# Kernel tuning notes

Measured on AMD Instinct MI355X. Metric: run time of the kernel, lower is better.

Reference implementation:

```python
import jax, jax.numpy as jnp
import numpy as np

HIDDEN = 1024
EMBED = HIDDEN // 4
SEQ = 512
BATCH = 256
NUM_CLASSES = 10


def setup_inputs() -> dict:
    key = jax.random.key(0)
    ks = jax.random.split(key, 16)

    def w(k, d1, d2):
        # kaiming_normal_ with nonlinearity='linear': std = 1/sqrt(fan_in=d2)
        return jax.random.normal(k, (d1, d2), dtype=jnp.float32) / jnp.sqrt(d2)

    inp = {
        "x": jax.random.randint(ks[0], (BATCH, SEQ), 0, 3),
        "emb": jax.random.normal(ks[1], (3, EMBED), dtype=jnp.float32),
        "w_gx": w(ks[2], EMBED, HIDDEN), "w_gh": w(ks[3], HIDDEN, HIDDEN), "b_g": jnp.zeros((HIDDEN,), jnp.float32),
        "w_ix": w(ks[4], EMBED, HIDDEN), "w_ih": w(ks[5], HIDDEN, HIDDEN), "b_i": jnp.zeros((HIDDEN,), jnp.float32),
        "w_fx": w(ks[6], EMBED, HIDDEN), "w_fh": w(ks[7], HIDDEN, HIDDEN), "b_f": jnp.zeros((HIDDEN,), jnp.float32),
        "w_ox": w(ks[8], EMBED, HIDDEN), "w_oh": w(ks[9], HIDDEN, HIDDEN), "b_o": jnp.zeros((HIDDEN,), jnp.float32),
        "w_ph": w(ks[10], HIDDEN, NUM_CLASSES), "b_p": jnp.zeros((NUM_CLASSES,), jnp.float32),
    }
    return inp


def reference(x, emb, w_gx, w_gh, b_g, w_ix, w_ih, b_i, w_fx, w_fh, b_f,
              w_ox, w_oh, b_o, w_ph, b_p):
    B, T = x.shape
    embedded = emb[x]                         # [B, T, E]
    pad = ((x + 1) // 2).astype(emb.dtype)    # [B, T]

    xs = (jnp.swapaxes(embedded, 0, 1),       # [T, B, E]
          jnp.swapaxes(pad, 0, 1))            # [T, B]

    h0 = jnp.zeros((B, w_gh.shape[0]), emb.dtype)
    c0 = jnp.zeros_like(h0)

    def step(carry, inputs):
        h, c = carry
        xt, pt = inputs
        g = jnp.tanh(xt @ w_gx + h @ w_gh + b_g)
        i = jax.nn.sigmoid(xt @ w_ix + h @ w_ih + b_i)
        f = jax.nn.sigmoid(xt @ w_fx + h @ w_fh + b_f)
        o = jax.nn.sigmoid(xt @ w_ox + h @ w_oh + b_o)
        c = g * i + c * f
        h = jnp.tanh(c) * o
        c = c * pt[:, None]
        return (h, c), None

    (h, _), _ = jax.lax.scan(step, (h0, c0), xs)
    p = h @ w_ph + b_p                        # [B, num_classes]
    # Faithful to original: log_softmax over dim=0 (batch dim)
    return jax.nn.log_softmax(p, axis=0)
```

## Files before the change

kernel.cpp:

```cpp
#include <hip/hip_runtime.h>
#include <hip/hip_bf16.h>

#define T_SEQ 512
#define BATCH 256
#define HID   1024
#define EMBD  256
#define NCLS  10

typedef __bf16 bf16x8 __attribute__((ext_vector_type(8)));
typedef float  floatx16 __attribute__((ext_vector_type(16)));
typedef float  floatx2 __attribute__((ext_vector_type(2)));
typedef unsigned short ushortx8 __attribute__((ext_vector_type(8)));

__device__ __forceinline__ unsigned int f2bf(float f) {
    unsigned int u = __builtin_bit_cast(unsigned int, f);
    u += 0x7fffu + ((u >> 16) & 1u);
    return u >> 16;
}
__device__ __forceinline__ float sig_fast(float x) {
    return __builtin_amdgcn_rcpf(1.0f + __expf(-x));
}
__device__ __forceinline__ float tanh_fast(float x) {
    return 1.0f - 2.0f * __builtin_amdgcn_rcpf(1.0f + __expf(2.0f * x));
}

__global__ void prep_xw_kernel(const float* __restrict__ emb,
                               const float* __restrict__ wgx, const float* __restrict__ wix,
                               const float* __restrict__ wfx, const float* __restrict__ wox,
                               const float* __restrict__ bg,  const float* __restrict__ bi,
                               const float* __restrict__ bf,  const float* __restrict__ bo,
                               float* __restrict__ XW) {
    int gid = blockIdx.x * blockDim.x + threadIdx.x;
    if (gid >= 3 * 4 * HID) return;
    int tok  = gid >> 12;
    int gate = (gid >> 10) & 3;
    int n    = gid & 1023;
    const float* W = gate == 0 ? wgx : gate == 1 ? wix : gate == 2 ? wfx : wox;
    const float* B = gate == 0 ? bg  : gate == 1 ? bi  : gate == 2 ? bf  : bo;
    float acc = B[n];
    const float* e = emb + tok * EMBD;
    for (int k = 0; k < EMBD; ++k) acc += e[k] * W[k * HID + n];
    XW[gid] = acc;
}

__global__ void prep_w_kernel(const float* __restrict__ wgh, const float* __restrict__ wih,
                              const float* __restrict__ wfh, const float* __restrict__ woh,
                              unsigned short* __restrict__ Wt) {
    int bid = blockIdx.x;
    int w   = bid & 31;
    int i   = (bid >> 5) & 15;
    int q   = (bid >> 9) & 3;
    int g   = bid >> 11;
    const float* W = g == 0 ? wgh : g == 1 ? wih : g == 2 ? wfh : woh;
    int lane = threadIdx.x;
    int j    = w * 32 + (lane & 31);
    int k0   = q * 256 + i * 16 + (lane >> 5) * 8;
    ushortx8 o8;
    #pragma unroll
    for (int e = 0; e < 8; ++e) o8[e] = (unsigned short)f2bf(W[(k0 + e) * HID + j]);
    int frag = ((w * 4 + g) * 4 + q) * 16 + i;
    *(ushortx8*)&Wt[frag * 512 + lane * 8] = o8;
}

__global__ __launch_bounds__(512, 2)
void lstm_kernel(const int* __restrict__ x, const float* __restrict__ XW,
                 const unsigned short* __restrict__ Wt,
                 unsigned int* __restrict__ hbuf32, int* __restrict__ flags,
                 int* __restrict__ xflag) {
    __shared__ __align__(16) unsigned short hs[4 * 8448];
    __shared__ float gbuf[16 * 1152];
    __shared__ float xwl[384];
    __shared__ unsigned char xtokp[4096];
    __shared__ int qctr[4];
    __shared__ int use_local_sh;

    const int tid  = threadIdx.x;
    const int grp  = blockIdx.x & 7;
    const int w    = blockIdx.x >> 3;
    const int wv   = tid >> 6;
    const int qv   = wv >> 1;
    const int pv   = wv & 1;
    const int lane = tid & 63;
    const int m32  = lane & 31;
    const int hv5  = lane >> 5;

    {
        int xcc = 0;
        asm volatile("s_getreg_b32 %0, hwreg(HW_REG_XCC_ID)" : "=s"(xcc));
        if (tid == 0) {
            __hip_atomic_store(&xflag[grp * 32 + w], xcc + 1, __ATOMIC_RELAXED,
                               __HIP_MEMORY_SCOPE_SYSTEM);
        }
        if (wv == 0) {
            int v;
            for (;;) {
                v = __hip_atomic_load(&xflag[grp * 32 + (lane & 31)], __ATOMIC_RELAXED,
                                      __HIP_MEMORY_SCOPE_SYSTEM);
                if (__all(v != 0)) break;
                __builtin_amdgcn_s_sleep(2);
            }
            int v0 = __shfl(v, 0, 64);
            if (lane == 0) use_local_sh = __all(v == v0) ? 1 : 0;
        }
    }

    bf16x8 Bf0[16], Bf1[16];
    {
        const unsigned short* wb0 = Wt + (size_t)(((w * 4 + 2 * pv + 0) * 4 + qv) * 16) * 512
                                       + (size_t)lane * 8;
        const unsigned short* wb1 = Wt + (size_t)(((w * 4 + 2 * pv + 1) * 4 + qv) * 16) * 512
                                       + (size_t)lane * 8;
        #pragma unroll
        for (int i = 0; i < 16; ++i) {
            Bf0[i] = *(const bf16x8*)(wb0 + i * 512);
            Bf1[i] = *(const bf16x8*)(wb1 + i * 512);
        }
    }
    if (tid < 384) {
        int tok = tid >> 7, g = (tid >> 5) & 3, jl = tid & 31;
        xwl[tid] = XW[(tok * 4 + g) * HID + w * 32 + jl];
    }
    for (int i = tid; i < 4096; i += 512) {
        int row = i >> 7, b = i & 127;
        const int* xr = &x[(grp * 32 + row) * T_SEQ + b * 4];
        xtokp[i] = (unsigned char)((xr[0] & 3) | ((xr[1] & 3) << 2)
                                   | ((xr[2] & 3) << 4) | ((xr[3] & 3) << 6));
    }
    if (tid < 4) qctr[tid] = 0;
    __syncthreads();
    const bool use_local = (use_local_sh != 0);

    const int erow = tid >> 4;
    const int jc2  = tid & 15;
    float cst[2] = {0.f, 0.f};
    unsigned long long* hs64 = (unsigned long long*)hs;

    for (int s = 0; s < T_SEQ; ++s) {
        if (s > 0) {
            const int fidx = grp * 32 + qv * 8 + (lane & 7);
            if (use_local) {
                for (;;) {
                    int v = __hip_atomic_load(&flags[fidx], __ATOMIC_RELAXED,
                                              __HIP_MEMORY_SCOPE_AGENT);
                    if (__all(v >= s)) break;
                    __builtin_amdgcn_s_sleep(1);
                }
            } else {
                for (;;) {
                    int v = __hip_atomic_load(&flags[fidx], __ATOMIC_RELAXED,
                                              __HIP_MEMORY_SCOPE_SYSTEM);
                    if (__all(v >= s)) break;
                    __builtin_amdgcn_s_sleep(1);
                }
            }
        }

        {
            const unsigned long long* hp64 = (const unsigned long long*)
                (hbuf32 + (size_t)(s & 1) * (BATCH * HID / 2));
            unsigned long long tmp[16];
            #pragma unroll
            for (int it = 0; it < 16; ++it) {
                int flat = it * 64 + lane;
                int row  = pv * 16 + (flat >> 6);
                int c4   = flat & 63;
                const unsigned long long* src =
                    &hp64[(size_t)(grp * 32 + row) * 256 + qv * 64 + c4];
                tmp[it] = use_local
                    ? __hip_atomic_load(src, __ATOMIC_RELAXED, __HIP_MEMORY_SCOPE_AGENT)
                    : __hip_atomic_load(src, __ATOMIC_RELAXED, __HIP_MEMORY_SCOPE_SYSTEM);
            }
            #pragma unroll
            for (int it = 0; it < 16; ++it) {
                int flat = it * 64 + lane;
                int row  = pv * 16 + (flat >> 6);
                int c4   = flat & 63;
                hs64[qv * 2112 + row * 66 + c4] = tmp[it];
            }
        }
        {
            if (lane == 0)
                __hip_atomic_fetch_add(&qctr[qv], 1, __ATOMIC_ACQ_REL,
                                       __HIP_MEMORY_SCOPE_WORKGROUP);
            const int target = 2 * (s + 1);
            while (__hip_atomic_load(&qctr[qv], __ATOMIC_ACQUIRE,
                                     __HIP_MEMORY_SCOPE_WORKGROUP) < target)
                __builtin_amdgcn_s_sleep(0);
        }

        floatx16 acc0 = {0.f,0.f,0.f,0.f,0.f,0.f,0.f,0.f,0.f,0.f,0.f,0.f,0.f,0.f,0.f,0.f};
        floatx16 acc1 = acc0;
        const unsigned short* ap = hs + qv * 8448 + m32 * 264 + hv5 * 8;
        #pragma unroll
        for (int i = 0; i < 16; ++i) {
            bf16x8 a = *(const bf16x8*)(ap + i * 16);
            acc0 = __builtin_amdgcn_mfma_f32_32x32x16_bf16(a, Bf0[i], acc0, 0, 0, 0);
            acc1 = __builtin_amdgcn_mfma_f32_32x32x16_bf16(a, Bf1[i], acc1, 0, 0, 0);
        }

        {
            float* gb0 = &gbuf[(size_t)((2 * pv + 0) * 4 + qv) * 1152];
            float* gb1 = &gbuf[(size_t)((2 * pv + 1) * 4 + qv) * 1152];
            #pragma unroll
            for (int reg = 0; reg < 16; ++reg) {
                int row = (reg & 3) + 8 * (reg >> 2) + 4 * hv5;
                gb0[row * 36 + m32] = acc0[reg];
                gb1[row * 36 + m32] = acc1[reg];
            }
        }
        __syncthreads();

        {
            int byte = xtokp[erow * 128 + (s >> 2)];
            int tk   = (byte >> ((s & 3) * 2)) & 3;
            const float* xb = &xwl[tk * 128];
            const int go = erow * 36 + jc2 * 2;
            floatx2 ag, ai, af, ao;
            #define SUMQ(dst, g) dst = *(const floatx2*)&gbuf[((g)*4+0)*1152 + go] \
                                     + *(const floatx2*)&gbuf[((g)*4+1)*1152 + go] \
                                     + *(const floatx2*)&gbuf[((g)*4+2)*1152 + go] \
                                     + *(const floatx2*)&gbuf[((g)*4+3)*1152 + go]
            SUMQ(ag, 0); SUMQ(ai, 1); SUMQ(af, 2); SUMQ(ao, 3);
            #undef SUMQ
            floatx2 xg = *(const floatx2*)&xb[0 * 32 + jc2 * 2];
            floatx2 xi = *(const floatx2*)&xb[1 * 32 + jc2 * 2];
            floatx2 xf = *(const floatx2*)&xb[2 * 32 + jc2 * 2];
            floatx2 xo = *(const floatx2*)&xb[3 * 32 + jc2 * 2];
            unsigned int hvv[2];
            #pragma unroll
            for (int u = 0; u < 2; ++u) {
                float g  = tanh_fast(ag[u] + xg[u]);
                float ii = sig_fast(ai[u] + xi[u]);
                float ff = sig_fast(af[u] + xf[u]);
                float oo = sig_fast(ao[u] + xo[u]);
                float cn = g * ii + cst[u] * ff;
                float h  = tanh_fast(cn) * oo;
                cst[u]   = (tk != 0) ? cn : 0.0f;
                hvv[u]   = f2bf(h);
            }
            unsigned int* hnext = hbuf32 + (size_t)((s + 1) & 1) * (BATCH * HID / 2);
            unsigned int* hp = &hnext[((grp * 32 + erow) * HID + w * 32 + jc2 * 2) >> 1];
            unsigned int hval = hvv[0] | (hvv[1] << 16);
            if (use_local) {
                __hip_atomic_store(hp, hval, __ATOMIC_RELAXED, __HIP_MEMORY_SCOPE_WORKGROUP);
            } else {
                __hip_atomic_store(hp, hval, __ATOMIC_RELAXED, __HIP_MEMORY_SCOPE_SYSTEM);
            }
        }
        __syncthreads();

        if (s < T_SEQ - 1 && tid == 0) {
            if (use_local) {
                __hip_atomic_store(&flags[grp * 32 + w], s + 1,
                                   __ATOMIC_RELAXED, __HIP_MEMORY_SCOPE_WORKGROUP);
            } else {
                __hip_atomic_store(&flags[grp * 32 + w], s + 1,
                                   __ATOMIC_RELAXED, __HIP_MEMORY_SCOPE_SYSTEM);
            }
        }
    }
}

__global__ void proj_kernel(const unsigned short* __restrict__ h,
                            const float* __restrict__ wph, const float* __restrict__ bp,
                            float* __restrict__ out) {
    __shared__ float wl[HID * NCLS];
    __shared__ float red[256];
    int tid = threadIdx.x;
    for (int i = tid; i < HID * NCLS; i += 256) wl[i] = wph[i];
    __syncthreads();
    float p[NCLS];
    #pragma unroll
    for (int c2 = 0; c2 < NCLS; ++c2) p[c2] = bp[c2];
    const unsigned short* hr = h + tid * HID;
    for (int k0 = 0; k0 < HID / 8; ++k0) {
        bf16x8 hv = *(const bf16x8*)(hr + k0 * 8);
        #pragma unroll
        for (int j = 0; j < 8; ++j) {
            float hk = (float)hv[j];
            #pragma unroll
            for (int c2 = 0; c2 < NCLS; ++c2) p[c2] += hk * wl[(k0 * 8 + j) * NCLS + c2];
        }
    }
    for (int c2 = 0; c2 < NCLS; ++c2) {
        red[tid] = p[c2];
        __syncthreads();
        for (int s = 128; s > 0; s >>= 1) {
            if (tid < s) red[tid] = fmaxf(red[tid], red[tid + s]);
            __syncthreads();
        }
        float mx = red[0];
        __syncthreads();
        red[tid] = __expf(p[c2] - mx);
        __syncthreads();
        for (int s = 128; s > 0; s >>= 1) {
            if (tid < s) red[tid] += red[tid + s];
            __syncthreads();
        }
        float lse = mx + __logf(red[0]);
        __syncthreads();
        out[tid * NCLS + c2] = p[c2] - lse;
    }
}

extern "C" void kernel_launch(void* const* d_in, const int* in_sizes, int n_in,
                              void* d_out, int out_size, void* d_ws, size_t ws_size,
                              hipStream_t stream) {
    const int*   x    = (const int*)d_in[0];
    const float* emb  = (const float*)d_in[1];
    const float* wgx  = (const float*)d_in[2];
    const float* wgh  = (const float*)d_in[3];
    const float* bg_  = (const float*)d_in[4];
    const float* wix  = (const float*)d_in[5];
    const float* wih  = (const float*)d_in[6];
    const float* bi_  = (const float*)d_in[7];
    const float* wfx  = (const float*)d_in[8];
    const float* wfh  = (const float*)d_in[9];
    const float* bf_  = (const float*)d_in[10];
    const float* wox  = (const float*)d_in[11];
    const float* woh  = (const float*)d_in[12];
    const float* bo_  = (const float*)d_in[13];
    const float* wph  = (const float*)d_in[14];
    const float* bp_  = (const float*)d_in[15];
    float* out = (float*)d_out;

    char* wsp = (char*)d_ws;
    int*            flags = (int*)wsp;
    int*            xflag = (int*)(wsp + 4096);
    float*          XW    = (float*)(wsp + 8192);
    unsigned short* Wt    = (unsigned short*)(wsp + 8192 + 49152);
    unsigned int*   hbuf32= (unsigned int*)(wsp + 8192 + 49152 + 8388608);

    hipMemsetAsync(flags, 0, 8192, stream);
    hipMemsetAsync(hbuf32, 0, BATCH * HID * sizeof(unsigned short), stream);

    prep_xw_kernel<<<48, 256, 0, stream>>>(emb, wgx, wix, wfx, wox,
                                           bg_, bi_, bf_, bo_, XW);
    prep_w_kernel<<<8192, 64, 0, stream>>>(wgh, wih, wfh, woh, Wt);

    void* args[] = { (void*)&x, (void*)&XW, (void*)&Wt, (void*)&hbuf32,
                     (void*)&flags, (void*)&xflag };
    hipError_t cerr = hipLaunchCooperativeKernel((void*)lstm_kernel, dim3(256), dim3(512),
                                                 args, 0, stream);
    if (cerr != hipSuccess) {
        lstm_kernel<<<dim3(256), dim3(512), 0, stream>>>(x, XW, Wt, hbuf32, flags, xflag);
    }

    proj_kernel<<<1, 256, 0, stream>>>((const unsigned short*)hbuf32, wph, bp_, out);
}
```

Measured before the change: 1.879 ms.

## Restructure LSTM block to 4 waves each holding all four gate weight slices

Each block now runs 4 waves instead of 8. Each wave keeps the bf16 recurrent weights for all four gates of its K-quarter in registers, so one shared h tile feeds four MFMA chains. The per-quarter LDS counter barrier is replaced by an lgkmcnt wait. Per-wave flag increments replace the block-level flag store, and input-projection values move from LDS into registers selected by packed tokens. The epilogue now handles 4 batch rows per thread with a transposed gate buffer. The aim is less intra-block synchronisation and fewer waves per step, at the cost of higher register pressure and less latency hiding.

```diff
diff --git a/kernel.cpp b/kernel.cpp
--- a/kernel.cpp
+++ b/kernel.cpp
@@ -9,7 +9,7 @@
 
 typedef __bf16 bf16x8 __attribute__((ext_vector_type(8)));
 typedef float  floatx16 __attribute__((ext_vector_type(16)));
-typedef float  floatx2 __attribute__((ext_vector_type(2)));
+typedef float  floatx4 __attribute__((ext_vector_type(4)));
 typedef unsigned short ushortx8 __attribute__((ext_vector_type(8)));
 
 __device__ __forceinline__ unsigned int f2bf(float f) {
@@ -62,24 +62,20 @@
     *(ushortx8*)&Wt[frag * 512 + lane * 8] = o8;
 }
 
-__global__ __launch_bounds__(512, 2)
+__global__ __launch_bounds__(256, 1)
 void lstm_kernel(const int* __restrict__ x, const float* __restrict__ XW,
                  const unsigned short* __restrict__ Wt,
                  unsigned int* __restrict__ hbuf32, int* __restrict__ flags,
                  int* __restrict__ xflag) {
-    __shared__ __align__(16) unsigned short hs[4 * 8448];
-    __shared__ float gbuf[16 * 1152];
-    __shared__ float xwl[384];
+    __shared__ __align__(16) unsigned short hs[4][32][264];
+    __shared__ __align__(16) float gbufT[16][32][36];
     __shared__ unsigned char xtokp[4096];
-    __shared__ int qctr[4];
     __shared__ int use_local_sh;
 
     const int tid  = threadIdx.x;
     const int grp  = blockIdx.x & 7;
     const int w    = blockIdx.x >> 3;
-    const int wv   = tid >> 6;
-    const int qv   = wv >> 1;
-    const int pv   = wv & 1;
+    const int q    = tid >> 6;
     const int lane = tid & 63;
     const int m32  = lane & 31;
     const int hv5  = lane >> 5;
@@ -91,7 +87,7 @@
             __hip_atomic_store(&xflag[grp * 32 + w], xcc + 1, __ATOMIC_RELAXED,
                                __HIP_MEMORY_SCOPE_SYSTEM);
         }
-        if (wv == 0) {
+        if (q == 0) {
             int v;
             for (;;) {
                 v = __hip_atomic_load(&xflag[grp * 32 + (lane & 31)], __ATOMIC_RELAXED,
@@ -104,52 +100,57 @@
         }
     }
 
-    bf16x8 Bf0[16], Bf1[16];
-    {
-        const unsigned short* wb0 = Wt + (size_t)(((w * 4 + 2 * pv + 0) * 4 + qv) * 16) * 512
-                                       + (size_t)lane * 8;
-        const unsigned short* wb1 = Wt + (size_t)(((w * 4 + 2 * pv + 1) * 4 + qv) * 16) * 512
-                                       + (size_t)lane * 8;
-        #pragma unroll
-        for (int i = 0; i < 16; ++i) {
-            Bf0[i] = *(const bf16x8*)(wb0 + i * 512);
-            Bf1[i] = *(const bf16x8*)(wb1 + i * 512);
-        }
-    }
-    if (tid < 384) {
-        int tok = tid >> 7, g = (tid >> 5) & 3, jl = tid & 31;
-        xwl[tid] = XW[(tok * 4 + g) * HID + w * 32 + jl];
-    }
-    for (int i = tid; i < 4096; i += 512) {
-        int row = i >> 7, b = i & 127;
-        const int* xr = &x[(grp * 32 + row) * T_SEQ + b * 4];
-        xtokp[i] = (unsigned char)((xr[0] & 3) | ((xr[1] & 3) << 2)
-                                   | ((xr[2] & 3) << 4) | ((xr[3] & 3) << 6));
-    }
-    if (tid < 4) qctr[tid] = 0;
+    bf16x8 Bf[4][16];
+    #pragma unroll
+    for (int g = 0; g < 4; ++g) {
+        const unsigned short* wb = Wt + (size_t)(((w * 4 + g) * 4 + q) * 16) * 512
+                                      + (size_t)lane * 8;
+        #pragma unroll
+        for (int i = 0; i < 16; ++i)
+            Bf[g][i] = *(const bf16x8*)(wb + i * 512);
+    }
+
+    const int c  = tid & 31;
+    const int rb = (tid >> 5) * 4;
+
+    float xw0[4], xw1[4], xw2[4];
+    #pragma unroll
+    for (int g = 0; g < 4; ++g) {
+        xw0[g] = XW[(0 * 4 + g) * HID + w * 32 + c];
+        xw1[g] = XW[(1 * 4 + g) * HID + w * 32 + c];
+        xw2[g] = XW[(2 * 4 + g) * HID + w * 32 + c];
+    }
+
+    for (int i = tid; i < 4096; i += 256) {
+        int s_ = i >> 3, blk = i & 7;
+        int t0 = x[(grp * 32 + blk * 4 + 0) * T_SEQ + s_] & 3;
+        int t1 = x[(grp * 32 + blk * 4 + 1) * T_SEQ + s_] & 3;
+        int t2 = x[(grp * 32 + blk * 4 + 2) * T_SEQ + s_] & 3;
+        int t3 = x[(grp * 32 + blk * 4 + 3) * T_SEQ + s_] & 3;
+        xtokp[i] = (unsigned char)(t0 | (t1 << 2) | (t2 << 4) | (t3 << 6));
+    }
     __syncthreads();
     const bool use_local = (use_local_sh != 0);
 
-    const int erow = tid >> 4;
-    const int jc2  = tid & 15;
-    float cst[2] = {0.f, 0.f};
-    unsigned long long* hs64 = (unsigned long long*)hs;
+    float cst[4] = {0.f, 0.f, 0.f, 0.f};
+    unsigned long long* hsq = (unsigned long long*)&hs[q][0][0];
 
     for (int s = 0; s < T_SEQ; ++s) {
         if (s > 0) {
-            const int fidx = grp * 32 + qv * 8 + (lane & 7);
+            const int fidx = grp * 32 + q * 8 + (lane & 7);
+            const int target = 4 * s;
             if (use_local) {
                 for (;;) {
                     int v = __hip_atomic_load(&flags[fidx], __ATOMIC_RELAXED,
                                               __HIP_MEMORY_SCOPE_AGENT);
-                    if (__all(v >= s)) break;
+                    if (__all(v >= target)) break;
                     __builtin_amdgcn_s_sleep(1);
                 }
             } else {
                 for (;;) {
                     int v = __hip_atomic_load(&flags[fidx], __ATOMIC_RELAXED,
                                               __HIP_MEMORY_SCOPE_SYSTEM);
-                    if (__all(v >= s)) break;
+                    if (__all(v >= target)) break;
                     __builtin_amdgcn_s_sleep(1);
                 }
             }
@@ -158,106 +159,104 @@
         {
             const unsigned long long* hp64 = (const unsigned long long*)
                 (hbuf32 + (size_t)(s & 1) * (BATCH * HID / 2));
-            unsigned long long tmp[16];
             #pragma unroll
-            for (int it = 0; it < 16; ++it) {
-                int flat = it * 64 + lane;
-                int row  = pv * 16 + (flat >> 6);
-                int c4   = flat & 63;
-                const unsigned long long* src =
-                    &hp64[(size_t)(grp * 32 + row) * 256 + qv * 64 + c4];
-                tmp[it] = use_local
-                    ? __hip_atomic_load(src, __ATOMIC_RELAXED, __HIP_MEMORY_SCOPE_AGENT)
-                    : __hip_atomic_load(src, __ATOMIC_RELAXED, __HIP_MEMORY_SCOPE_SYSTEM);
-            }
-            #pragma unroll
-            for (int it = 0; it < 16; ++it) {
-                int flat = it * 64 + lane;
-                int row  = pv * 16 + (flat >> 6);
-                int c4   = flat & 63;
-                hs64[qv * 2112 + row * 66 + c4] = tmp[it];
-            }
-        }
-        {
-            if (lane == 0)
-                __hip_atomic_fetch_add(&qctr[qv], 1, __ATOMIC_ACQ_REL,
-                                       __HIP_MEMORY_SCOPE_WORKGROUP);
-            const int target = 2 * (s + 1);
-            while (__hip_atomic_load(&qctr[qv], __ATOMIC_ACQUIRE,
-                                     __HIP_MEMORY_SCOPE_WORKGROUP) < target)
-                __builtin_amdgcn_s_sleep(0);
-        }
-
-        floatx16 acc0 = {0.f,0.f,0.f,0.f,0.f,0.f,0.f,0.f,0.f,0.f,0.f,0.f,0.f,0.f,0.f,0.f};
-        floatx16 acc1 = acc0;
-        const unsigned short* ap = hs + qv * 8448 + m32 * 264 + hv5 * 8;
+            for (int half = 0; half < 2; ++half) {
+                unsigned long long tmp[16];
+                #pragma unroll
+                for (int it = 0; it < 16; ++it) {
+                    int chunk = (half * 16 + it) * 64 + lane;
+                    int r  = chunk >> 6;
+                    int kq = chunk & 63;
+                    const unsigned long long* src =
+                        &hp64[(size_t)(grp * 32 + r) * 256 + q * 64 + kq];
+                    tmp[it] = use_local
+                        ? __hip_atomic_load(src, __ATOMIC_RELAXED, __HIP_MEMORY_SCOPE_AGENT)
+                        : __hip_atomic_load(src, __ATOMIC_RELAXED, __HIP_MEMORY_SCOPE_SYSTEM);
+                }
+                #pragma unroll
+                for (int it = 0; it < 16; ++it) {
+                    int chunk = (half * 16 + it) * 64 + lane;
+                    int r  = chunk >> 6;
+                    int kq = chunk & 63;
+                    hsq[r * 66 + kq] = tmp[it];
+                }
+            }
+        }
+        asm volatile("s_waitcnt lgkmcnt(0)" ::: "memory");
+
+        floatx16 acc[4];
+        #pragma unroll
+        for (int g = 0; g < 4; ++g) acc[g] = (floatx16)(0.f);
+        const unsigned short* ap = &hs[q][m32][hv5 * 8];
         #pragma unroll
         for (int i = 0; i < 16; ++i) {
             bf16x8 a = *(const bf16x8*)(ap + i * 16);
-            acc0 = __builtin_amdgcn_mfma_f32_32x32x16_bf16(a, Bf0[i], acc0, 0, 0, 0);
-            acc1 = __builtin_amdgcn_mfma_f32_32x32x16_bf16(a, Bf1[i], acc1, 0, 0, 0);
-        }
+            acc[0] = __builtin_amdgcn_mfma_f32_32x32x16_bf16(a, Bf[0][i], acc[0], 0, 0, 0);
+            acc[1] = __builtin_amdgcn_mfma_f32_32x32x16_bf16(a, Bf[1][i], acc[1], 0, 0, 0);
+            acc[2] = __builtin_amdgcn_mfma_f32_32x32x16_bf16(a, Bf[2][i], acc[2], 0, 0, 0);
+            acc[3] = __builtin_amdgcn_mfma_f32_32x32x16_bf16(a, Bf[3][i], acc[3], 0, 0, 0);
+        }
+
+        #pragma unroll
+        for (int g = 0; g < 4; ++g) {
+            #pragma unroll
+            for (int rr = 0; rr < 4; ++rr) {
+                floatx4 v = { acc[g][4 * rr + 0], acc[g][4 * rr + 1],
+                              acc[g][4 * rr + 2], acc[g][4 * rr + 3] };
+                *(floatx4*)&gbufT[g * 4 + q][m32][8 * rr + 4 * hv5] = v;
+            }
+        }
+        __syncthreads();
 
         {
-            float* gb0 = &gbuf[(size_t)((2 * pv + 0) * 4 + qv) * 1152];
-            float* gb1 = &gbuf[(size_t)((2 * pv + 1) * 4 + qv) * 1152];
+            int byte = xtokp[s * 8 + (tid >> 5)];
+            floatx4 ag = *(const floatx4*)&gbufT[0][c][rb] + *(const floatx4*)&gbufT[1][c][rb]
+                       + *(const floatx4*)&gbufT[2][c][rb] + *(const floatx4*)&gbufT[3][c][rb];
+            floatx4 ai = *(const floatx4*)&gbufT[4][c][rb] + *(const floatx4*)&gbufT[5][c][rb]
+                       + *(const floatx4*)&gbufT[6][c][rb] + *(const floatx4*)&gbufT[7][c][rb];
+            floatx4 af = *(const floatx4*)&gbufT[8][c][rb] + *(const floatx4*)&gbufT[9][c][rb]
+                       + *(const floatx4*)&gbufT[10][c][rb] + *(const floatx4*)&gbufT[11][c][rb];
+            floatx4 ao = *(const floatx4*)&gbufT[12][c][rb] + *(const floatx4*)&gbufT[13][c][rb]
+                       + *(const floatx4*)&gbufT[14][c][rb] + *(const floatx4*)&gbufT[15][c][rb];
+            unsigned short* hnext = (unsigned short*)
+                (hbuf32 + (size_t)((s + 1) & 1) * (BATCH * HID / 2));
             #pragma unroll
-            for (int reg = 0; reg < 16; ++reg) {
-                int row = (reg & 3) + 8 * (reg >> 2) + 4 * hv5;
-                gb0[row * 36 + m32] = acc0[reg];
-                gb1[row * 36 + m32] = acc1[reg];
-            }
-        }
-        __syncthreads();
-
-        {
-            int byte = xtokp[erow * 128 + (s >> 2)];
-            int tk   = (byte >> ((s & 3) * 2)) & 3;
-            const float* xb = &xwl[tk * 128];
-            const int go = erow * 36 + jc2 * 2;
-            floatx2 ag, ai, af, ao;
-            #define SUMQ(dst, g) dst = *(const floatx2*)&gbuf[((g)*4+0)*1152 + go] \
-                                     + *(const floatx2*)&gbuf[((g)*4+1)*1152 + go] \
-                                     + *(const floatx2*)&gbuf[((g)*4+2)*1152 + go] \
-                                     + *(const floatx2*)&gbuf[((g)*4+3)*1152 + go]
-            SUMQ(ag, 0); SUMQ(ai, 1); SUMQ(af, 2); SUMQ(ao, 3);
-            #undef SUMQ
-            floatx2 xg = *(const floatx2*)&xb[0 * 32 + jc2 * 2];
-            floatx2 xi = *(const floatx2*)&xb[1 * 32 + jc2 * 2];
-            floatx2 xf = *(const floatx2*)&xb[2 * 32 + jc2 * 2];
-            floatx2 xo = *(const floatx2*)&xb[3 * 32 + jc2 * 2];
-            unsigned int hvv[2];
-            #pragma unroll
-            for (int u = 0; u < 2; ++u) {
-                float g  = tanh_fast(ag[u] + xg[u]);
-                float ii = sig_fast(ai[u] + xi[u]);
-                float ff = sig_fast(af[u] + xf[u]);
-                float oo = sig_fast(ao[u] + xo[u]);
-                float cn = g * ii + cst[u] * ff;
+            for (int i = 0; i < 4; ++i) {
+                int tk = (byte >> (2 * i)) & 3;
+                float xg = tk == 0 ? xw0[0] : (tk == 1 ? xw1[0] : xw2[0]);
+                float xi = tk == 0 ? xw0[1] : (tk == 1 ? xw1[1] : xw2[1]);
+                float xf = tk == 0 ? xw0[2] : (tk == 1 ? xw1[2] : xw2[2]);
+                float xo = tk == 0 ? xw0[3] : (tk == 1 ? xw1[3] : xw2[3]);
+                float g  = tanh_fast(ag[i] + xg);
+                float ii = sig_fast(ai[i] + xi);
+                float ff = sig_fast(af[i] + xf);
+                float oo = sig_fast(ao[i] + xo);
+                float cn = g * ii + cst[i] * ff;
                 float h  = tanh_fast(cn) * oo;
-                cst[u]   = (tk != 0) ? cn : 0.0f;
-                hvv[u]   = f2bf(h);
-            }
-            unsigned int* hnext = hbuf32 + (size_t)((s + 1) & 1) * (BATCH * HID / 2);
-            unsigned int* hp = &hnext[((grp * 32 + erow) * HID + w * 32 + jc2 * 2) >> 1];
-            unsigned int hval = hvv[0] | (hvv[1] << 16);
-            if (use_local) {
-                __hip_atomic_store(hp, hval, __ATOMIC_RELAXED, __HIP_MEMORY_SCOPE_WORKGROUP);
-            } else {
-                __hip_atomic_store(hp, hval, __ATOMIC_RELAXED, __HIP_MEMORY_SCOPE_SYSTEM);
-            }
-        }
-        __syncthreads();
-
-        if (s < T_SEQ - 1 && tid == 0) {
-            if (use_local) {
-                __hip_atomic_store(&flags[grp * 32 + w], s + 1,
-                                   __ATOMIC_RELAXED, __HIP_MEMORY_SCOPE_WORKGROUP);
-            } else {
-                __hip_atomic_store(&flags[grp * 32 + w], s + 1,
-                                   __ATOMIC_RELAXED, __HIP_MEMORY_SCOPE_SYSTEM);
-            }
-        }
+                cst[i]   = (tk != 0) ? cn : 0.0f;
+                unsigned short hv = (unsigned short)f2bf(h);
+                unsigned short* hp = &hnext[(size_t)(grp * 32 + rb + i) * HID + w * 32 + c];
+                if (use_local) {
+                    __hip_atomic_store(hp, hv, __ATOMIC_RELAXED, __HIP_MEMORY_SCOPE_WORKGROUP);
+                } else {
+                    __hip_atomic_store(hp, hv, __ATOMIC_RELAXED, __HIP_MEMORY_SCOPE_SYSTEM);
+                }
+            }
+        }
+
+        if (s < T_SEQ - 1) {
+            asm volatile("s_waitcnt vmcnt(0)" ::: "memory");
+            if (lane == 0) {
+                if (use_local) {
+                    __hip_atomic_fetch_add(&flags[grp * 32 + w], 1, __ATOMIC_RELAXED,
+                                           __HIP_MEMORY_SCOPE_AGENT);
+                } else {
+                    __hip_atomic_fetch_add(&flags[grp * 32 + w], 1, __ATOMIC_RELEASE,
+                                           __HIP_MEMORY_SCOPE_SYSTEM);
+                }
+            }
+        }
+        __syncthreads();
     }
 }
 
@@ -340,10 +339,10 @@
 
     void* args[] = { (void*)&x, (void*)&XW, (void*)&Wt, (void*)&hbuf32,
                      (void*)&flags, (void*)&xflag };
-    hipError_t cerr = hipLaunchCooperativeKernel((void*)lstm_kernel, dim3(256), dim3(512),
+    hipError_t cerr = hipLaunchCooperativeKernel((void*)lstm_kernel, dim3(256), dim3(256),
                                                  args, 0, stream);
     if (cerr != hipSuccess) {
-        lstm_kernel<<<dim3(256), dim3(512), 0, stream>>>(x, XW, Wt, hbuf32, flags, xflag);
+        lstm_kernel<<<dim3(256), dim3(256), 0, stream>>>(x, XW, Wt, hbuf32, flags, xflag);
     }
 
     proj_kernel<<<1, 256, 0, stream>>>((const unsigned short*)hbuf32, wph, bp_, out);
```

Result: slower. 4.243 ms (+125.8%).
